# Optimization experiments

Measured on AMD Instinct MI355X. Metric: run time of the kernel, lower is better.

The kernel has to match this reference:

```python
import jax, jax.numpy as jnp
import numpy as np

NEG_SLOPE = 0.01

def setup_inputs() -> dict:
    key = jax.random.key(0)
    ks = jax.random.split(key, 6)
    B, N, IN, OUT = 4, 4096, 256, 128
    x = jax.random.normal(ks[0], (B, N, IN), dtype=jnp.float32)
    # fc: Linear(in, out, bias=False); attn_l/attn_r: Linear(out, 1) with bias
    W_fc = jax.random.normal(ks[1], (IN, OUT), dtype=jnp.float32) / np.sqrt(IN)
    w_l = jax.random.normal(ks[2], (OUT,), dtype=jnp.float32) / np.sqrt(OUT)
    b_l = jax.random.normal(ks[3], (), dtype=jnp.float32) * 0.01
    w_r = jax.random.normal(ks[4], (OUT,), dtype=jnp.float32) / np.sqrt(OUT)
    b_r = jax.random.normal(ks[5], (), dtype=jnp.float32) * 0.01
    return {"x": x, "W_fc": W_fc, "w_l": w_l, "b_l": b_l, "w_r": w_r, "b_r": b_r}

def reference(x, W_fc, w_l, b_l, w_r, b_r):
    # feats: [B, N, OUT]
    feats = jnp.einsum('bni,io->bno', x, W_fc)
    f1 = jnp.einsum('bno,o->bn', feats, w_l) + b_l  # [B, N]
    f2 = jnp.einsum('bno,o->bn', feats, w_r) + b_r  # [B, N]
    # logits[b, i, j] = f1[b, i] + f2[b, j]  (broadcast-add)
    logits = f1[:, :, None] + f2[:, None, :]        # [B, N, N]
    scores = jnp.where(logits >= 0, logits, NEG_SLOPE * logits)
    coefs = jax.nn.softmax(scores, axis=1)          # softmax over dim=1, as in torch code
    return jnp.einsum('bij,bjo->bio', coefs, feats) # [B, N, OUT]
```

## Files before the change

### kernel.cpp

```cpp
#include <hip/hip_runtime.h>

using u16 = unsigned short;
using u32 = unsigned int;
using u64 = unsigned long long;

typedef short bf16x8 __attribute__((ext_vector_type(8)));
typedef float f32x4 __attribute__((ext_vector_type(4)));

static constexpr int NB  = 4;
static constexpr int NN  = 4096;
static constexpr int KIN = 256;
static constexpr int FO  = 128;
static constexpr int NROW = NB * NN;
static constexpr int NCC = 64;
static constexpr float SLOPE = 0.01f;

__device__ __forceinline__ u16 f2bf(float f) {
  const u32 u = __float_as_uint(f);
  return (u16)((u + 0x7fffu + ((u >> 16) & 1u)) >> 16);
}
__device__ __forceinline__ float bf2f(u16 h) {
  return __uint_as_float(((u32)h) << 16);
}
__device__ __forceinline__ float dot4(const float4& a, const float4& b) {
  return a.x * b.x + a.y * b.y + a.z * b.z + a.w * b.w;
}

__device__ __forceinline__ u32 f2key(float f) {
  const u32 b = __float_as_uint(f);
  return (b & 0x80000000u) ? ~b : (b | 0x80000000u);
}
__device__ __forceinline__ float key2f(u32 u) {
  const u32 b = (u & 0x80000000u) ? (u ^ 0x80000000u) : ~u;
  return __uint_as_float(b);
}

__device__ __forceinline__ u64 shfl_xor64(u64 v, int m) {
  const u32 lo = __shfl_xor((u32)(v & 0xffffffffu), m, 64);
  const u32 hi = __shfl_xor((u32)(v >> 32), m, 64);
  return ((u64)hi << 32) | (u64)lo;
}
__device__ __forceinline__ void cswap(u64& a, u64& b, bool up) {
  if ((a > b) == up) { const u64 tmp = a; a = b; b = tmp; }
}

__device__ __forceinline__ void reg_session(u64 e[4], int t, int k) {
  const int jstart = (k > 256) ? 128 : (k >> 1);
  for (int j = jstart; j >= 4; j >>= 1) {
    const int J = j >> 2;
    const bool up   = ((t & (k >> 2)) == 0);
    const bool lowr = ((t & J) == 0);
#pragma unroll
    for (int r = 0; r < 4; ++r) {
      const u64 o = shfl_xor64(e[r], J);
      const bool less = e[r] < o;
      e[r] = ((lowr == up) == less) ? e[r] : o;
    }
  }
  if (k >= 4) {
    const bool up = ((t & (k >> 2)) == 0);
    cswap(e[0], e[2], up); cswap(e[1], e[3], up);
  }
  {
    const bool up0 = (((4 * t)     & k) == 0);
    const bool up1 = (((4 * t + 2) & k) == 0);
    cswap(e[0], e[1], up0); cswap(e[2], e[3], up1);
  }
}

__global__ __launch_bounds__(256) void k0_prep(const float* __restrict__ W,
                                               const float* __restrict__ wl,
                                               const float* __restrict__ wr,
                                               float* __restrict__ u_l,
                                               float* __restrict__ u_r,
                                               u16* __restrict__ whT,
                                               u16* __restrict__ wloT) {
  const int t = threadIdx.x;
  const int blk = blockIdx.x;
  if (blk < 64) {
    const int k = blk * 4 + (t >> 6);
    const int lane = t & 63;
    const float w0 = W[k * FO + lane], w1 = W[k * FO + 64 + lane];
    float a1 = w0 * wl[lane] + w1 * wl[64 + lane];
    float a2 = w0 * wr[lane] + w1 * wr[64 + lane];
#pragma unroll
    for (int off = 1; off < 64; off <<= 1) {
      a1 += __shfl_xor(a1, off, 64);
      a2 += __shfl_xor(a2, off, 64);
    }
    if (lane == 0) { u_l[k] = a1; u_r[k] = a2; }
  } else {
#pragma unroll
    for (int e = 0; e < 2; ++e) {
      const int idx = (blk - 64) * 512 + t + e * 256;
      const int col = idx >> 8, k = idx & 255;
      const float v = W[k * FO + col];
      const u16 h = f2bf(v);
      whT[col * KIN + k]  = h;
      wloT[col * KIN + k] = f2bf(v - bf2f(h));
    }
  }
}

__global__ __launch_bounds__(256) void k1_fused(const float* __restrict__ x,
                                                const u16* __restrict__ whT,
                                                const u16* __restrict__ wloT,
                                                const float* __restrict__ u_l,
                                                const float* __restrict__ u_r,
                                                const float* __restrict__ blp,
                                                const float* __restrict__ brp,
                                                float* __restrict__ feats,
                                                float* __restrict__ f1g,
                                                float* __restrict__ f2g) {
  __shared__ u16 axh[64][72];
  __shared__ u16 axl[64][72];
  __shared__ u16 bwh[128][72];
  __shared__ u16 bwl[128][72];
  const int t = threadIdx.x;
  const int w = t >> 6, lane = t & 63;
  const int wm = w >> 1, wn = w & 1;
  const int row0 = blockIdx.x * 64;
  const int xr = t >> 3, xc = t & 7;
  f32x4 acc[2][4];
#pragma unroll
  for (int m = 0; m < 2; ++m)
#pragma unroll
    for (int n = 0; n < 4; ++n) acc[m][n] = (f32x4)0.f;

  float d1a = 0.f, d2a = 0.f, d1b = 0.f, d2b = 0.f;
  float4 xa0, xa1, xb0, xb1;
  bf16x8 wh_[4], wl_[4];

  {
    const float* pa = x + (size_t)(row0 + xr) * KIN + xc * 8;
    const float* pb = x + (size_t)(row0 + xr + 32) * KIN + xc * 8;
    xa0 = *(const float4*)pa; xa1 = *(const float4*)(pa + 4);
    xb0 = *(const float4*)pb; xb1 = *(const float4*)(pb + 4);
#pragma unroll
    for (int i = 0; i < 4; ++i) {
      const int v = t + i * 256;
      const int col = v >> 3, c = v & 7;
      wh_[i] = *(const bf16x8*)(whT + (size_t)col * KIN + c * 8);
      wl_[i] = *(const bf16x8*)(wloT + (size_t)col * KIN + c * 8);
    }
  }

  for (int it = 0; it < 4; ++it) {
    if (it) __syncthreads();
    {
      const float4 ul0 = *(const float4*)(u_l + it * 64 + xc * 8);
      const float4 ul1 = *(const float4*)(u_l + it * 64 + xc * 8 + 4);
      const float4 ur0 = *(const float4*)(u_r + it * 64 + xc * 8);
      const float4 ur1 = *(const float4*)(u_r + it * 64 + xc * 8 + 4);
      d1a += dot4(xa0, ul0) + dot4(xa1, ul1);
      d2a += dot4(xa0, ur0) + dot4(xa1, ur1);
      d1b += dot4(xb0, ul0) + dot4(xb1, ul1);
      d2b += dot4(xb0, ur0) + dot4(xb1, ur1);
    }
    {
      float va[8] = {xa0.x, xa0.y, xa0.z, xa0.w, xa1.x, xa1.y, xa1.z, xa1.w};
      float vb[8] = {xb0.x, xb0.y, xb0.z, xb0.w, xb1.x, xb1.y, xb1.z, xb1.w};
      bf16x8 ha, la, hb, lb;
#pragma unroll
      for (int q = 0; q < 8; ++q) {
        const u16 h1 = f2bf(va[q]);
        ha[q] = (short)h1; la[q] = (short)f2bf(va[q] - bf2f(h1));
        const u16 h2 = f2bf(vb[q]);
        hb[q] = (short)h2; lb[q] = (short)f2bf(vb[q] - bf2f(h2));
      }
      *(bf16x8*)(&axh[xr][xc * 8]) = ha;
      *(bf16x8*)(&axl[xr][xc * 8]) = la;
      *(bf16x8*)(&axh[xr + 32][xc * 8]) = hb;
      *(bf16x8*)(&axl[xr + 32][xc * 8]) = lb;
    }
#pragma unroll
    for (int i = 0; i < 4; ++i) {
      const int v = t + i * 256;
      const int col = v >> 3, c = v & 7;
      *(bf16x8*)(&bwh[col][c * 8]) = wh_[i];
      *(bf16x8*)(&bwl[col][c * 8]) = wl_[i];
    }
    __syncthreads();
    if (it < 3) {
      const float* pa = x + (size_t)(row0 + xr) * KIN + (it + 1) * 64 + xc * 8;
      const float* pb = x + (size_t)(row0 + xr + 32) * KIN + (it + 1) * 64 + xc * 8;
      xa0 = *(const float4*)pa; xa1 = *(const float4*)(pa + 4);
      xb0 = *(const float4*)pb; xb1 = *(const float4*)(pb + 4);
#pragma unroll
      for (int i = 0; i < 4; ++i) {
        const int v = t + i * 256;
        const int col = v >> 3, c = v & 7;
        wh_[i] = *(const bf16x8*)(whT + (size_t)col * KIN + (it + 1) * 64 + c * 8);
        wl_[i] = *(const bf16x8*)(wloT + (size_t)col * KIN + (it + 1) * 64 + c * 8);
      }
    }
#pragma unroll
    for (int kk = 0; kk < 2; ++kk) {
      const int kb = kk * 32 + (lane >> 4) * 8;
      bf16x8 ah[2], al[2], bh[4], blo[4];
#pragma unroll
      for (int m = 0; m < 2; ++m) {
        const int r = wm * 32 + m * 16 + (lane & 15);
        ah[m] = *(const bf16x8*)(&axh[r][kb]);
        al[m] = *(const bf16x8*)(&axl[r][kb]);
      }
#pragma unroll
      for (int n = 0; n < 4; ++n) {
        const int cidx = wn * 64 + n * 16 + (lane & 15);
        bh[n]  = *(const bf16x8*)(&bwh[cidx][kb]);
        blo[n] = *(const bf16x8*)(&bwl[cidx][kb]);
      }
#pragma unroll
      for (int m = 0; m < 2; ++m)
#pragma unroll
        for (int n = 0; n < 4; ++n) {
          acc[m][n] = __builtin_amdgcn_mfma_f32_16x16x32_bf16(ah[m], bh[n],  acc[m][n], 0, 0, 0);
          acc[m][n] = __builtin_amdgcn_mfma_f32_16x16x32_bf16(ah[m], blo[n], acc[m][n], 0, 0, 0);
          acc[m][n] = __builtin_amdgcn_mfma_f32_16x16x32_bf16(al[m], bh[n],  acc[m][n], 0, 0, 0);
        }
    }
  }

#pragma unroll
  for (int m = 0; m < 2; ++m) {
    const int rb = row0 + wm * 32 + m * 16 + (lane >> 4) * 4;
    const int cb = wn * 64 + (lane & 15);
#pragma unroll
    for (int n = 0; n < 4; ++n)
#pragma unroll
      for (int r = 0; r < 4; ++r)
        feats[(size_t)(rb + r) * FO + cb + n * 16] = acc[m][n][r];
  }

#pragma unroll
  for (int off = 1; off < 8; off <<= 1) {
    d1a += __shfl_xor(d1a, off, 64);
    d2a += __shfl_xor(d2a, off, 64);
    d1b += __shfl_xor(d1b, off, 64);
    d2b += __shfl_xor(d2b, off, 64);
  }
  if ((t & 7) == 0) {
    const float bl = blp[0], br = brp[0];
    f1g[row0 + xr] = d1a + bl;
    f2g[row0 + xr] = d2a + br;
    f1g[row0 + xr + 32] = d1b + bl;
    f2g[row0 + xr + 32] = d2b + br;
  }
}

__global__ __launch_bounds__(1024, 1) void k3a_sort(const float* __restrict__ f1g,
                                                    const float* __restrict__ f2g,
                                                    float* __restrict__ f1sort,
                                                    float* __restrict__ sc1,
                                                    float* __restrict__ sc2,
                                                    float* __restrict__ f2sort,
                                                    int* __restrict__ jidxS) {
  __shared__ u64 lds[NN];
  __shared__ float wsumA[16], wsumB[16];
  const int t = threadIdx.x;
  const int lane = t & 63, wv = t >> 6;
  const int b = blockIdx.x & 3;
  const int task = blockIdx.x >> 2;
  const int base = b * NN;
  const float* __restrict__ src = task ? f2g : f1g;

  u64 e[4];
#pragma unroll
  for (int r = 0; r < 4; ++r) {
    const int i = 4 * t + r;
    e[r] = ((u64)f2key(src[base + i]) << 32) | (u32)i;
  }

  for (int k = 2; k <= 256; k <<= 1) reg_session(e, t, k);
#pragma unroll
  for (int r = 0; r < 4; ++r) lds[4 * t + r] = e[r];
  __syncthreads();

  for (int k = 512; k <= NN; k <<= 1) {
    for (int j = k >> 1; j >= 256; j >>= 1) {
#pragma unroll
      for (int pp = 0; pp < 2; ++pp) {
        const int p = t + pp * 1024;
        const int i = ((p & ~(j - 1)) << 1) | (p & (j - 1));
        const int ix = i | j;
        const bool up = ((i & k) == 0);
        const u64 a = lds[i], c = lds[ix];
        if ((a > c) == up) { lds[i] = c; lds[ix] = a; }
      }
      __syncthreads();
    }
#pragma unroll
    for (int r = 0; r < 4; ++r) e[r] = lds[4 * t + r];
    reg_session(e, t, k);
    if (k < NN) {
#pragma unroll
      for (int r = 0; r < 4; ++r) lds[4 * t + r] = e[r];
      __syncthreads();
    }
  }

  if (task == 0) {
    float kf[4], a[4], c[4];
#pragma unroll
    for (int r = 0; r < 4; ++r) {
      kf[r] = key2f((u32)(e[r] >> 32));
      f1sort[base + 4 * t + r] = kf[r];
      a[r] = expf(kf[r]);
      c[r] = expf(SLOPE * kf[r]);
    }
#pragma unroll
    for (int r = 1; r < 4; ++r) { a[r] += a[r - 1]; c[r] += c[r - 1]; }
    const float sa = a[3], sb = c[3];
    float pa = sa, pb = sb;
    for (int off = 1; off < 64; off <<= 1) {
      const float oa = __shfl_up(pa, off, 64);
      const float ob = __shfl_up(pb, off, 64);
      if (lane >= off) { pa += oa; pb += ob; }
    }
    if (lane == 63) { wsumA[wv] = pa; wsumB[wv] = pb; }
    __syncthreads();
    float wpa = 0.f, wpb = 0.f;
    for (int w2 = 0; w2 < wv; ++w2) { wpa += wsumA[w2]; wpb += wsumB[w2]; }
    const float basea = wpa + pa - sa, baseb = wpb + pb - sb;
#pragma unroll
    for (int r = 0; r < 4; ++r) {
      sc1[base + 4 * t + r] = basea + a[r];
      sc2[base + 4 * t + r] = baseb + c[r];
    }
  } else {
#pragma unroll
    for (int r = 0; r < 4; ++r) {
      f2sort[base + 4 * t + r] = key2f((u32)(e[r] >> 32));
      jidxS[base + 4 * t + r]  = (int)(e[r] & 0xffffffffu);
    }
  }
}

__device__ __forceinline__ int lower_bound_s(const float* a, int n, float t) {
  int lo = 0, hi = n;
  while (lo < hi) {
    const int mid = (lo + hi) >> 1;
    if (a[mid] < t) lo = mid + 1; else hi = mid;
  }
  return lo;
}

__global__ __launch_bounds__(512) void k3b_ab(const float* __restrict__ f1sort,
                                              const float* __restrict__ sc1,
                                              const float* __restrict__ sc2,
                                              const float* __restrict__ f2sort,
                                              const float* __restrict__ f1g,
                                              float* __restrict__ alphaS,
                                              float* __restrict__ betaS,
                                              int* __restrict__ kposA,
                                              float* __restrict__ E1g,
                                              float* __restrict__ E2g) {
  __shared__ float s_f1[NN];
  __shared__ float s_f2[NN];
  const int b = blockIdx.x >> 3;
  const int part = blockIdx.x & 7;
  const int base = b * NN;
  for (int i = threadIdx.x; i < NN; i += 512) {
    s_f1[i] = f1sort[base + i];
    s_f2[i] = f2sort[base + i];
  }
  __syncthreads();
  const int g = part * 512 + threadIdx.x;
  const float T1 = sc1[base + NN - 1];
  const float f1max = s_f1[NN - 1];
  {
    const float f2v = s_f2[g];
    const float m = f1max + f2v;
    const float M = (m >= 0.f) ? m : SLOPE * m;
    const int p = lower_bound_s(s_f1, NN, -f2v);
    const float S1 = T1 - (p > 0 ? sc1[base + p - 1] : 0.f);
    const float S2 = (p > 0 ? sc2[base + p - 1] : 0.f);
    const float ea = expf(f2v - M);
    const float eb = expf(SLOPE * f2v - M);
    const float invD = 1.0f / (ea * S1 + eb * S2);
    alphaS[base + g] = ea * invD;
    betaS[base + g]  = eb * invD;
  }
  {
    const float f1v = f1g[base + g];
    kposA[base + g] = lower_bound_s(s_f2, NN, -f1v);
    E1g[base + g] = expf(f1v);
    E2g[base + g] = expf(SLOPE * f1v);
  }
}

__global__ __launch_bounds__(128) void k4a_pref(const float* __restrict__ feats,
                                                const float* __restrict__ alphaS,
                                                const float* __restrict__ betaS,
                                                const int* __restrict__ jidxS,
                                                float* __restrict__ finePreA,
                                                float* __restrict__ finePreB) {
  const int b = blockIdx.x >> 6, cc = blockIdx.x & 63;
  const int o = threadIdx.x;
  const int base = b * NN + cc * 64;
  const float* fb = feats + (size_t)b * NN * FO;
  float accA = 0.f, accB = 0.f;
#pragma unroll 8
  for (int q = 0; q < 64; ++q) {
    const int kk = base + q;
    const int j = jidxS[kk];
    const float fv = fb[(size_t)j * FO + o];
    accA = fmaf(alphaS[kk], fv, accA);
    accB = fmaf(betaS[kk], fv, accB);
    finePreA[(size_t)kk * FO + o] = accA;
    finePreB[(size_t)kk * FO + o] = accB;
  }
}

__global__ __launch_bounds__(128) void k4c_coar(const float* __restrict__ finePreA,
                                                const float* __restrict__ finePreB,
                                                float* __restrict__ coarA,
                                                float* __restrict__ coarB) {
  const int b = blockIdx.x;
  const int o = threadIdx.x;
  float runA = 0.f, runB = 0.f;
#pragma unroll
  for (int c = 0; c < NCC; ++c) {
    coarA[(size_t)(b * (NCC + 1) + c) * FO + o] = runA;
    coarB[(size_t)(b * (NCC + 1) + c) * FO + o] = runB;
    runA += finePreA[(size_t)(b * NN + c * 64 + 63) * FO + o];
    runB += finePreB[(size_t)(b * NN + c * 64 + 63) * FO + o];
  }
  coarA[(size_t)(b * (NCC + 1) + NCC) * FO + o] = runA;
  coarB[(size_t)(b * (NCC + 1) + NCC) * FO + o] = runB;
}

__global__ __launch_bounds__(256) void k5_out(const float* __restrict__ finePreA,
                                              const float* __restrict__ finePreB,
                                              const float* __restrict__ coarA,
                                              const float* __restrict__ coarB,
                                              const int* __restrict__ kposA,
                                              const float* __restrict__ E1g,
                                              const float* __restrict__ E2g,
                                              float* __restrict__ out) {
  const int t = threadIdx.x;
  const int row = blockIdx.x * 2 + (t >> 7);
  const int o = t & 127;
  const int b = row >> 12;
  const int kp = kposA[row];
  const float e1 = E1g[row], e2 = E2g[row];
  const int c = kp >> 6;

  float runA = coarA[(size_t)(b * (NCC + 1) + c) * FO + o];
  float runB = coarB[(size_t)(b * (NCC + 1) + c) * FO + o];
  const float totA = coarA[(size_t)(b * (NCC + 1) + NCC) * FO + o];
  if (kp & 63) {
    runA += finePreA[(size_t)(b * NN + kp - 1) * FO + o];
    runB += finePreB[(size_t)(b * NN + kp - 1) * FO + o];
  }
  out[(size_t)row * FO + o] = fmaf(e1, totA - runA, e2 * runB);
}

extern "C" void kernel_launch(void* const* d_in, const int* in_sizes, int n_in,
                              void* d_out, int out_size, void* d_ws, size_t ws_size,
                              hipStream_t stream) {
  const float* x  = (const float*)d_in[0];
  const float* W  = (const float*)d_in[1];
  const float* wl = (const float*)d_in[2];
  const float* bl = (const float*)d_in[3];
  const float* wr = (const float*)d_in[4];
  const float* br = (const float*)d_in[5];
  float* out = (float*)d_out;

  float* ws = (float*)d_ws;
  float* feats    = ws; ws += NROW * FO;
  float* finePreA = ws; ws += NROW * FO;
  float* finePreB = ws; ws += NROW * FO;
  float* f1g      = ws; ws += NROW;
  float* f2g      = ws; ws += NROW;
  float* f1sort   = ws; ws += NROW;
  float* f2sort   = ws; ws += NROW;
  float* sc1      = ws; ws += NROW;
  float* sc2      = ws; ws += NROW;
  float* alphaS   = ws; ws += NROW;
  float* betaS    = ws; ws += NROW;
  float* E1g      = ws; ws += NROW;
  float* E2g      = ws; ws += NROW;
  int* jidxS      = (int*)ws; ws += NROW;
  int* kposA      = (int*)ws; ws += NROW;
  float* coarA    = ws; ws += NB * (NCC + 1) * FO;
  float* coarB    = ws; ws += NB * (NCC + 1) * FO;
  float* u_l      = ws; ws += KIN;
  float* u_r      = ws; ws += KIN;
  u16* whT  = (u16*)ws; ws += FO * KIN / 2;
  u16* wloT = (u16*)ws; ws += FO * KIN / 2;
  (void)in_sizes; (void)n_in; (void)out_size; (void)ws_size;

  hipLaunchKernelGGL(k0_prep,  dim3(128),       dim3(256),  0, stream,
                     W, wl, wr, u_l, u_r, whT, wloT);
  hipLaunchKernelGGL(k1_fused, dim3(NROW / 64), dim3(256),  0, stream,
                     x, whT, wloT, u_l, u_r, bl, br, feats, f1g, f2g);
  hipLaunchKernelGGL(k3a_sort, dim3(8),         dim3(1024), 0, stream,
                     f1g, f2g, f1sort, sc1, sc2, f2sort, jidxS);
  hipLaunchKernelGGL(k3b_ab,   dim3(NB * 8),    dim3(512),  0, stream,
                     f1sort, sc1, sc2, f2sort, f1g, alphaS, betaS, kposA, E1g, E2g);
  hipLaunchKernelGGL(k4a_pref, dim3(NB * NCC),  dim3(128),  0, stream,
                     feats, alphaS, betaS, jidxS, finePreA, finePreB);
  hipLaunchKernelGGL(k4c_coar, dim3(NB),        dim3(128),  0, stream,
                     finePreA, finePreB, coarA, coarB);
  hipLaunchKernelGGL(k5_out,   dim3(NROW / 2),  dim3(256),  0, stream,
                     finePreA, finePreB, coarA, coarB, kposA, E1g, E2g, out);
}
```

Before: 68.51 us.

## Fuse alpha/beta search and coarse prefix into prefix-sum kernel via last-block atomic

Merges the k3b_ab kernel (binary searches and softmax-normalisation coefficients) and the k4c_coar coarse scan into k4a_pref. Alpha/beta are now kept in shared memory instead of round-tripping through global memory. The last block to finish per batch is detected with an atomic counter and threadfence, and it runs the coarse scan. This removes two launches and their global traffic, at the cost of binary searches reading global memory rather than LDS and a serial tail block per batch.

```diff
diff --git a/kernel.cpp b/kernel.cpp
--- a/kernel.cpp
+++ b/kernel.cpp
@@ -68,15 +68,26 @@
   }
 }
 
+__device__ __forceinline__ int lower_bound_g(const float* __restrict__ a, int n, float t) {
+  int lo = 0, hi = n;
+  while (lo < hi) {
+    const int mid = (lo + hi) >> 1;
+    if (a[mid] < t) lo = mid + 1; else hi = mid;
+  }
+  return lo;
+}
+
 __global__ __launch_bounds__(256) void k0_prep(const float* __restrict__ W,
                                                const float* __restrict__ wl,
                                                const float* __restrict__ wr,
                                                float* __restrict__ u_l,
                                                float* __restrict__ u_r,
                                                u16* __restrict__ whT,
-                                               u16* __restrict__ wloT) {
+                                               u16* __restrict__ wloT,
+                                               int* __restrict__ cnt) {
   const int t = threadIdx.x;
   const int blk = blockIdx.x;
+  if (blk == 0 && t < NB) cnt[t] = 0;
   if (blk < 64) {
     const int k = blk * 4 + (t >> 6);
     const int lane = t & 63;
@@ -336,98 +347,88 @@
   }
 }
 
-__device__ __forceinline__ int lower_bound_s(const float* a, int n, float t) {
-  int lo = 0, hi = n;
-  while (lo < hi) {
-    const int mid = (lo + hi) >> 1;
-    if (a[mid] < t) lo = mid + 1; else hi = mid;
-  }
-  return lo;
-}
-
-__global__ __launch_bounds__(512) void k3b_ab(const float* __restrict__ f1sort,
-                                              const float* __restrict__ sc1,
-                                              const float* __restrict__ sc2,
-                                              const float* __restrict__ f2sort,
-                                              const float* __restrict__ f1g,
-                                              float* __restrict__ alphaS,
-                                              float* __restrict__ betaS,
-                                              int* __restrict__ kposA,
-                                              float* __restrict__ E1g,
-                                              float* __restrict__ E2g) {
-  __shared__ float s_f1[NN];
-  __shared__ float s_f2[NN];
-  const int b = blockIdx.x >> 3;
-  const int part = blockIdx.x & 7;
-  const int base = b * NN;
-  for (int i = threadIdx.x; i < NN; i += 512) {
-    s_f1[i] = f1sort[base + i];
-    s_f2[i] = f2sort[base + i];
-  }
-  __syncthreads();
-  const int g = part * 512 + threadIdx.x;
-  const float T1 = sc1[base + NN - 1];
-  const float f1max = s_f1[NN - 1];
-  {
-    const float f2v = s_f2[g];
+__global__ __launch_bounds__(128) void k4a_pref(const float* __restrict__ feats,
+                                                const float* __restrict__ f1sort,
+                                                const float* __restrict__ sc1,
+                                                const float* __restrict__ sc2,
+                                                const float* __restrict__ f2sort,
+                                                const float* __restrict__ f1g,
+                                                const int* __restrict__ jidxS,
+                                                float* __restrict__ finePreA,
+                                                float* __restrict__ finePreB,
+                                                int* __restrict__ kposA,
+                                                float* __restrict__ E1g,
+                                                float* __restrict__ E2g,
+                                                float* __restrict__ coarA,
+                                                float* __restrict__ coarB,
+                                                int* __restrict__ cnt) {
+  __shared__ float sal[64], sbe[64];
+  __shared__ int s_last;
+  const int b = blockIdx.x >> 6, cc = blockIdx.x & 63;
+  const int tid = threadIdx.x;
+  const int bb = b * NN;
+  const int base = bb + cc * 64;
+
+  if (tid < 64) {
+    const int pos = cc * 64 + tid;
+    const float T1 = sc1[bb + NN - 1];
+    const float f1max = f1sort[bb + NN - 1];
+    const float f2v = f2sort[bb + pos];
     const float m = f1max + f2v;
     const float M = (m >= 0.f) ? m : SLOPE * m;
-    const int p = lower_bound_s(s_f1, NN, -f2v);
-    const float S1 = T1 - (p > 0 ? sc1[base + p - 1] : 0.f);
-    const float S2 = (p > 0 ? sc2[base + p - 1] : 0.f);
+    const int pp = lower_bound_g(f1sort + bb, NN, -f2v);
+    const float S1 = T1 - (pp > 0 ? sc1[bb + pp - 1] : 0.f);
+    const float S2 = (pp > 0 ? sc2[bb + pp - 1] : 0.f);
     const float ea = expf(f2v - M);
     const float eb = expf(SLOPE * f2v - M);
     const float invD = 1.0f / (ea * S1 + eb * S2);
-    alphaS[base + g] = ea * invD;
-    betaS[base + g]  = eb * invD;
-  }
+    sal[tid] = ea * invD;
+    sbe[tid] = eb * invD;
+  } else {
+    const int row = cc * 64 + (tid - 64);
+    const float f1v = f1g[bb + row];
+    kposA[bb + row] = lower_bound_g(f2sort + bb, NN, -f1v);
+    E1g[bb + row] = expf(f1v);
+    E2g[bb + row] = expf(SLOPE * f1v);
+  }
+  __syncthreads();
+
   {
-    const float f1v = f1g[base + g];
-    kposA[base + g] = lower_bound_s(s_f2, NN, -f1v);
-    E1g[base + g] = expf(f1v);
-    E2g[base + g] = expf(SLOPE * f1v);
-  }
-}
-
-__global__ __launch_bounds__(128) void k4a_pref(const float* __restrict__ feats,
-                                                const float* __restrict__ alphaS,
-                                                const float* __restrict__ betaS,
-                                                const int* __restrict__ jidxS,
-                                                float* __restrict__ finePreA,
-                                                float* __restrict__ finePreB) {
-  const int b = blockIdx.x >> 6, cc = blockIdx.x & 63;
-  const int o = threadIdx.x;
-  const int base = b * NN + cc * 64;
-  const float* fb = feats + (size_t)b * NN * FO;
-  float accA = 0.f, accB = 0.f;
+    const int o = tid;
+    const float* fb = feats + (size_t)b * NN * FO;
+    float accA = 0.f, accB = 0.f;
 #pragma unroll 8
-  for (int q = 0; q < 64; ++q) {
-    const int kk = base + q;
-    const int j = jidxS[kk];
-    const float fv = fb[(size_t)j * FO + o];
-    accA = fmaf(alphaS[kk], fv, accA);
-    accB = fmaf(betaS[kk], fv, accB);
-    finePreA[(size_t)kk * FO + o] = accA;
-    finePreB[(size_t)kk * FO + o] = accB;
-  }
-}
-
-__global__ __launch_bounds__(128) void k4c_coar(const float* __restrict__ finePreA,
-                                                const float* __restrict__ finePreB,
-                                                float* __restrict__ coarA,
-                                                float* __restrict__ coarB) {
-  const int b = blockIdx.x;
-  const int o = threadIdx.x;
-  float runA = 0.f, runB = 0.f;
-#pragma unroll
-  for (int c = 0; c < NCC; ++c) {
-    coarA[(size_t)(b * (NCC + 1) + c) * FO + o] = runA;
-    coarB[(size_t)(b * (NCC + 1) + c) * FO + o] = runB;
-    runA += finePreA[(size_t)(b * NN + c * 64 + 63) * FO + o];
-    runB += finePreB[(size_t)(b * NN + c * 64 + 63) * FO + o];
-  }
-  coarA[(size_t)(b * (NCC + 1) + NCC) * FO + o] = runA;
-  coarB[(size_t)(b * (NCC + 1) + NCC) * FO + o] = runB;
+    for (int q = 0; q < 64; ++q) {
+      const int kk = base + q;
+      const int j = jidxS[kk];
+      const float fv = fb[(size_t)j * FO + o];
+      accA = fmaf(sal[q], fv, accA);
+      accB = fmaf(sbe[q], fv, accB);
+      finePreA[(size_t)kk * FO + o] = accA;
+      finePreB[(size_t)kk * FO + o] = accB;
+    }
+  }
+
+  __syncthreads();
+  if (tid == 0) {
+    __threadfence();
+    s_last = (atomicAdd(&cnt[b], 1) == NCC - 1) ? 1 : 0;
+  }
+  __syncthreads();
+  if (s_last) {
+    __threadfence();
+    const int o = tid;
+    float runA = 0.f, runB = 0.f;
+#pragma unroll 8
+    for (int c = 0; c < NCC; ++c) {
+      coarA[(size_t)(b * (NCC + 1) + c) * FO + o] = runA;
+      coarB[(size_t)(b * (NCC + 1) + c) * FO + o] = runB;
+      runA += finePreA[(size_t)(b * NN + c * 64 + 63) * FO + o];
+      runB += finePreB[(size_t)(b * NN + c * 64 + 63) * FO + o];
+    }
+    coarA[(size_t)(b * (NCC + 1) + NCC) * FO + o] = runA;
+    coarB[(size_t)(b * (NCC + 1) + NCC) * FO + o] = runB;
+  }
 }
 
 __global__ __launch_bounds__(256) void k5_out(const float* __restrict__ finePreA,
@@ -477,8 +478,6 @@
   float* f2sort   = ws; ws += NROW;
   float* sc1      = ws; ws += NROW;
   float* sc2      = ws; ws += NROW;
-  float* alphaS   = ws; ws += NROW;
-  float* betaS    = ws; ws += NROW;
   float* E1g      = ws; ws += NROW;
   float* E2g      = ws; ws += NROW;
   int* jidxS      = (int*)ws; ws += NROW;
@@ -489,20 +488,18 @@
   float* u_r      = ws; ws += KIN;
   u16* whT  = (u16*)ws; ws += FO * KIN / 2;
   u16* wloT = (u16*)ws; ws += FO * KIN / 2;
+  int* cnt  = (int*)ws; ws += NB;
   (void)in_sizes; (void)n_in; (void)out_size; (void)ws_size;
 
   hipLaunchKernelGGL(k0_prep,  dim3(128),       dim3(256),  0, stream,
-                     W, wl, wr, u_l, u_r, whT, wloT);
+                     W, wl, wr, u_l, u_r, whT, wloT, cnt);
   hipLaunchKernelGGL(k1_fused, dim3(NROW / 64), dim3(256),  0, stream,
                      x, whT, wloT, u_l, u_r, bl, br, feats, f1g, f2g);
   hipLaunchKernelGGL(k3a_sort, dim3(8),         dim3(1024), 0, stream,
                      f1g, f2g, f1sort, sc1, sc2, f2sort, jidxS);
-  hipLaunchKernelGGL(k3b_ab,   dim3(NB * 8),    dim3(512),  0, stream,
-                     f1sort, sc1, sc2, f2sort, f1g, alphaS, betaS, kposA, E1g, E2g);
   hipLaunchKernelGGL(k4a_pref, dim3(NB * NCC),  dim3(128),  0, stream,
-                     feats, alphaS, betaS, jidxS, finePreA, finePreB);
-  hipLaunchKernelGGL(k4c_coar, dim3(NB),        dim3(128),  0, stream,
-                     finePreA, finePreB, coarA, coarB);
+                     feats, f1sort, sc1, sc2, f2sort, f1g, jidxS,
+                     finePreA, finePreB, kposA, E1g, E2g, coarA, coarB, cnt);
   hipLaunchKernelGGL(k5_out,   dim3(NROW / 2),  dim3(256),  0, stream,
                      finePreA, finePreB, coarA, coarB, kposA, E1g, E2g, out);
 }
```

Result: slower. 75.82 us (+10.7%).

## Fuse alpha/beta computation into prefix kernel and store prefix sums every fourth row

Applied to the files above, without the earlier changes.

Merges the alpha/beta and kpos computation kernel into the prefix-sum kernel, which now works on 32-row chunks across 512 blocks, each reloading the sorted f1/f2 arrays into shared memory. The fine prefix arrays are written only every fourth row, cutting their size and write traffic by four. The output kernel rebuilds the missing up to three residual terms by gathering feats directly, and computes the exp factors inline instead of reading stored ones. In exchange each block repeats the 32KB shared load, and the output kernel does extra irregular gathers.

```diff
diff --git a/kernel.cpp b/kernel.cpp
--- a/kernel.cpp
+++ b/kernel.cpp
@@ -12,7 +12,9 @@
 static constexpr int KIN = 256;
 static constexpr int FO  = 128;
 static constexpr int NROW = NB * NN;
-static constexpr int NCC = 64;
+static constexpr int NCC = 128;
+static constexpr int CH  = 32;
+static constexpr int NGB = NN / 4;
 static constexpr float SLOPE = 0.01f;
 
 __device__ __forceinline__ u16 f2bf(float f) {
@@ -66,6 +68,15 @@
     const bool up1 = (((4 * t + 2) & k) == 0);
     cswap(e[0], e[1], up0); cswap(e[2], e[3], up1);
   }
+}
+
+__device__ __forceinline__ int lower_bound_s(const float* a, int n, float t) {
+  int lo = 0, hi = n;
+  while (lo < hi) {
+    const int mid = (lo + hi) >> 1;
+    if (a[mid] < t) lo = mid + 1; else hi = mid;
+  }
+  return lo;
 }
 
 __global__ __launch_bounds__(256) void k0_prep(const float* __restrict__ W,
@@ -336,79 +347,77 @@
   }
 }
 
-__device__ __forceinline__ int lower_bound_s(const float* a, int n, float t) {
-  int lo = 0, hi = n;
-  while (lo < hi) {
-    const int mid = (lo + hi) >> 1;
-    if (a[mid] < t) lo = mid + 1; else hi = mid;
-  }
-  return lo;
-}
-
-__global__ __launch_bounds__(512) void k3b_ab(const float* __restrict__ f1sort,
-                                              const float* __restrict__ sc1,
-                                              const float* __restrict__ sc2,
-                                              const float* __restrict__ f2sort,
-                                              const float* __restrict__ f1g,
-                                              float* __restrict__ alphaS,
-                                              float* __restrict__ betaS,
-                                              int* __restrict__ kposA,
-                                              float* __restrict__ E1g,
-                                              float* __restrict__ E2g) {
+__global__ __launch_bounds__(128) void k4_pref(const float* __restrict__ feats,
+                                               const float* __restrict__ f1sort,
+                                               const float* __restrict__ sc1,
+                                               const float* __restrict__ sc2,
+                                               const float* __restrict__ f2sort,
+                                               const float* __restrict__ f1g,
+                                               const int* __restrict__ jidxS,
+                                               float* __restrict__ alphaS,
+                                               float* __restrict__ betaS,
+                                               int* __restrict__ kposA,
+                                               float* __restrict__ finePreA,
+                                               float* __restrict__ finePreB) {
   __shared__ float s_f1[NN];
   __shared__ float s_f2[NN];
-  const int b = blockIdx.x >> 3;
-  const int part = blockIdx.x & 7;
-  const int base = b * NN;
-  for (int i = threadIdx.x; i < NN; i += 512) {
-    s_f1[i] = f1sort[base + i];
-    s_f2[i] = f2sort[base + i];
+  __shared__ float sal[CH], sbe[CH];
+  const int b = blockIdx.x >> 7, cc = blockIdx.x & 127;
+  const int tid = threadIdx.x;
+  const int bb = b * NN;
+
+  {
+    const float4* s1 = (const float4*)(f1sort + bb);
+    const float4* s2 = (const float4*)(f2sort + bb);
+    float4* t1 = (float4*)s_f1;
+    float4* t2 = (float4*)s_f2;
+#pragma unroll
+    for (int i = 0; i < NN / 4 / 128; ++i) {
+      t1[tid + i * 128] = s1[tid + i * 128];
+      t2[tid + i * 128] = s2[tid + i * 128];
+    }
   }
   __syncthreads();
-  const int g = part * 512 + threadIdx.x;
-  const float T1 = sc1[base + NN - 1];
-  const float f1max = s_f1[NN - 1];
-  {
-    const float f2v = s_f2[g];
+
+  if (tid < CH) {
+    const int pos = cc * CH + tid;
+    const float T1 = sc1[bb + NN - 1];
+    const float f1max = s_f1[NN - 1];
+    const float f2v = s_f2[pos];
     const float m = f1max + f2v;
     const float M = (m >= 0.f) ? m : SLOPE * m;
-    const int p = lower_bound_s(s_f1, NN, -f2v);
-    const float S1 = T1 - (p > 0 ? sc1[base + p - 1] : 0.f);
-    const float S2 = (p > 0 ? sc2[base + p - 1] : 0.f);
+    const int pp = lower_bound_s(s_f1, NN, -f2v);
+    const float S1 = T1 - (pp > 0 ? sc1[bb + pp - 1] : 0.f);
+    const float S2 = (pp > 0 ? sc2[bb + pp - 1] : 0.f);
     const float ea = expf(f2v - M);
     const float eb = expf(SLOPE * f2v - M);
     const float invD = 1.0f / (ea * S1 + eb * S2);
-    alphaS[base + g] = ea * invD;
-    betaS[base + g]  = eb * invD;
-  }
-  {
-    const float f1v = f1g[base + g];
-    kposA[base + g] = lower_bound_s(s_f2, NN, -f1v);
-    E1g[base + g] = expf(f1v);
-    E2g[base + g] = expf(SLOPE * f1v);
-  }
-}
-
-__global__ __launch_bounds__(128) void k4a_pref(const float* __restrict__ feats,
-                                                const float* __restrict__ alphaS,
-                                                const float* __restrict__ betaS,
-                                                const int* __restrict__ jidxS,
-                                                float* __restrict__ finePreA,
-                                                float* __restrict__ finePreB) {
-  const int b = blockIdx.x >> 6, cc = blockIdx.x & 63;
-  const int o = threadIdx.x;
-  const int base = b * NN + cc * 64;
+    const float al = ea * invD, be = eb * invD;
+    sal[tid] = al; sbe[tid] = be;
+    alphaS[bb + pos] = al; betaS[bb + pos] = be;
+  } else if (tid < 2 * CH) {
+    const int row = cc * CH + (tid - CH);
+    const float f1v = f1g[bb + row];
+    kposA[bb + row] = lower_bound_s(s_f2, NN, -f1v);
+  }
+  __syncthreads();
+
+  const int o = tid;
+  const int base = bb + cc * CH;
+  const int gbase = b * NGB + cc * (CH / 4);
   const float* fb = feats + (size_t)b * NN * FO;
   float accA = 0.f, accB = 0.f;
 #pragma unroll 8
-  for (int q = 0; q < 64; ++q) {
+  for (int q = 0; q < CH; ++q) {
     const int kk = base + q;
     const int j = jidxS[kk];
     const float fv = fb[(size_t)j * FO + o];
-    accA = fmaf(alphaS[kk], fv, accA);
-    accB = fmaf(betaS[kk], fv, accB);
-    finePreA[(size_t)kk * FO + o] = accA;
-    finePreB[(size_t)kk * FO + o] = accB;
+    accA = fmaf(sal[q], fv, accA);
+    accB = fmaf(sbe[q], fv, accB);
+    if ((q & 3) == 3) {
+      finePreA[(size_t)(gbase + (q >> 2)) * FO + o] = accA;
+      finePreB[(size_t)(gbase + (q >> 2)) * FO + o] = accB;
+    }
   }
 }
 
@@ -419,39 +428,54 @@
   const int b = blockIdx.x;
   const int o = threadIdx.x;
   float runA = 0.f, runB = 0.f;
-#pragma unroll
+#pragma unroll 8
   for (int c = 0; c < NCC; ++c) {
     coarA[(size_t)(b * (NCC + 1) + c) * FO + o] = runA;
     coarB[(size_t)(b * (NCC + 1) + c) * FO + o] = runB;
-    runA += finePreA[(size_t)(b * NN + c * 64 + 63) * FO + o];
-    runB += finePreB[(size_t)(b * NN + c * 64 + 63) * FO + o];
+    runA += finePreA[(size_t)(b * NGB + c * (CH / 4) + (CH / 4) - 1) * FO + o];
+    runB += finePreB[(size_t)(b * NGB + c * (CH / 4) + (CH / 4) - 1) * FO + o];
   }
   coarA[(size_t)(b * (NCC + 1) + NCC) * FO + o] = runA;
   coarB[(size_t)(b * (NCC + 1) + NCC) * FO + o] = runB;
 }
 
-__global__ __launch_bounds__(256) void k5_out(const float* __restrict__ finePreA,
+__global__ __launch_bounds__(256) void k5_out(const float* __restrict__ feats,
+                                              const float* __restrict__ alphaS,
+                                              const float* __restrict__ betaS,
+                                              const int* __restrict__ jidxS,
+                                              const float* __restrict__ finePreA,
                                               const float* __restrict__ finePreB,
                                               const float* __restrict__ coarA,
                                               const float* __restrict__ coarB,
                                               const int* __restrict__ kposA,
-                                              const float* __restrict__ E1g,
-                                              const float* __restrict__ E2g,
+                                              const float* __restrict__ f1g,
                                               float* __restrict__ out) {
   const int t = threadIdx.x;
   const int row = blockIdx.x * 2 + (t >> 7);
   const int o = t & 127;
   const int b = row >> 12;
+  const int bb = b * NN;
   const int kp = kposA[row];
-  const float e1 = E1g[row], e2 = E2g[row];
-  const int c = kp >> 6;
+  const float f1v = f1g[row];
+  const float e1 = expf(f1v), e2 = expf(SLOPE * f1v);
+  const int c = kp >> 5;
 
   float runA = coarA[(size_t)(b * (NCC + 1) + c) * FO + o];
   float runB = coarB[(size_t)(b * (NCC + 1) + c) * FO + o];
   const float totA = coarA[(size_t)(b * (NCC + 1) + NCC) * FO + o];
-  if (kp & 63) {
-    runA += finePreA[(size_t)(b * NN + kp - 1) * FO + o];
-    runB += finePreB[(size_t)(b * NN + kp - 1) * FO + o];
+  const int gin = (kp >> 2) - c * (CH / 4);
+  if (gin > 0) {
+    runA += finePreA[(size_t)(b * NGB + c * (CH / 4) + gin - 1) * FO + o];
+    runB += finePreB[(size_t)(b * NGB + c * (CH / 4) + gin - 1) * FO + o];
+  }
+  const int res = kp & 3;
+  const float* fb = feats + (size_t)b * NN * FO;
+  for (int r = 0; r < res; ++r) {
+    const int q = bb + kp - res + r;
+    const int j = jidxS[q];
+    const float fv = fb[(size_t)j * FO + o];
+    runA = fmaf(alphaS[q], fv, runA);
+    runB = fmaf(betaS[q], fv, runB);
   }
   out[(size_t)row * FO + o] = fmaf(e1, totA - runA, e2 * runB);
 }
@@ -469,8 +493,8 @@
 
   float* ws = (float*)d_ws;
   float* feats    = ws; ws += NROW * FO;
-  float* finePreA = ws; ws += NROW * FO;
-  float* finePreB = ws; ws += NROW * FO;
+  float* finePreA = ws; ws += (NROW / 4) * FO;
+  float* finePreB = ws; ws += (NROW / 4) * FO;
   float* f1g      = ws; ws += NROW;
   float* f2g      = ws; ws += NROW;
   float* f1sort   = ws; ws += NROW;
@@ -479,8 +503,6 @@
   float* sc2      = ws; ws += NROW;
   float* alphaS   = ws; ws += NROW;
   float* betaS    = ws; ws += NROW;
-  float* E1g      = ws; ws += NROW;
-  float* E2g      = ws; ws += NROW;
   int* jidxS      = (int*)ws; ws += NROW;
   int* kposA      = (int*)ws; ws += NROW;
   float* coarA    = ws; ws += NB * (NCC + 1) * FO;
@@ -497,12 +519,12 @@
                      x, whT, wloT, u_l, u_r, bl, br, feats, f1g, f2g);
   hipLaunchKernelGGL(k3a_sort, dim3(8),         dim3(1024), 0, stream,
                      f1g, f2g, f1sort, sc1, sc2, f2sort, jidxS);
-  hipLaunchKernelGGL(k3b_ab,   dim3(NB * 8),    dim3(512),  0, stream,
-                     f1sort, sc1, sc2, f2sort, f1g, alphaS, betaS, kposA, E1g, E2g);
-  hipLaunchKernelGGL(k4a_pref, dim3(NB * NCC),  dim3(128),  0, stream,
-                     feats, alphaS, betaS, jidxS, finePreA, finePreB);
+  hipLaunchKernelGGL(k4_pref,  dim3(NB * NCC),  dim3(128),  0, stream,
+                     feats, f1sort, sc1, sc2, f2sort, f1g, jidxS,
+                     alphaS, betaS, kposA, finePreA, finePreB);
   hipLaunchKernelGGL(k4c_coar, dim3(NB),        dim3(128),  0, stream,
                      finePreA, finePreB, coarA, coarB);
   hipLaunchKernelGGL(k5_out,   dim3(NROW / 2),  dim3(256),  0, stream,
-                     finePreA, finePreB, coarA, coarB, kposA, E1g, E2g, out);
-}
+                     feats, alphaS, betaS, jidxS, finePreA, finePreB,
+                     coarA, coarB, kposA, f1g, out);
+}
```

Result: slower. 76.22 us (+11.3%).
